# Optimization experiments

Hardware: AMD Instinct MI355X
Metric: run time of the kernel (lower is better)

## Reference

```python
import jax, jax.numpy as jnp
import numpy as np

HEADS = 12
HEAD_SIZE = 64
HIDDEN = 768


def _rope_tables(seqlen, dim, dtype):
    inv_freq = 1.0 / (10000.0 ** (jnp.arange(0, dim, 2, dtype=jnp.float32) / dim))
    t = jnp.arange(seqlen, dtype=jnp.float32)
    freqs = t[:, None] * inv_freq[None, :]  # [L, dim/2]
    return jnp.sin(freqs).astype(dtype), jnp.cos(freqs).astype(dtype)


def _apply_rope(x, sin, cos):
    # x: [B, L, H, D]; sin/cos: [L, D/2] -> broadcast as [1, L, 1, D/2]
    sin = sin[None, :, None, :]
    cos = cos[None, :, None, :]
    x1 = x[..., 0::2]
    x2 = x[..., 1::2]
    out1 = x1 * cos - x2 * sin
    out2 = x1 * sin + x2 * cos
    # interleave back: stack on new last axis then flatten
    return jnp.stack([out1, out2], axis=-1).reshape(x.shape)


def setup_inputs() -> dict:
    key = jax.random.key(0)
    k1, k2, k3 = jax.random.split(key, 3)
    B, L = 8, 512
    inputs = jax.random.normal(k1, (B, L, HIDDEN), dtype=jnp.float32)
    attention_mask = jnp.ones((B, L), dtype=jnp.int32)
    out_dim = HEADS * 2 * HEAD_SIZE
    W = jax.random.normal(k2, (HIDDEN, out_dim), dtype=jnp.float32) * (1.0 / np.sqrt(HIDDEN))
    b = jax.random.normal(k3, (out_dim,), dtype=jnp.float32) * 0.02
    return {"inputs": inputs, "W": W, "b": b, "attention_mask": attention_mask}


def reference(inputs, W, b, attention_mask):
    B, L, _ = inputs.shape
    x = inputs @ W + b  # [B, L, H*2*D]
    x = x.reshape(B, L, HEADS, 2, HEAD_SIZE)
    qw = x[..., 0, :]  # [B, L, H, D]
    kw = x[..., 1, :]
    sin, cos = _rope_tables(L, HEAD_SIZE, x.dtype)
    qw = _apply_rope(qw, sin, cos)
    kw = _apply_rope(kw, sin, cos)
    logits = jnp.einsum('bmhd,bnhd->bhmn', qw, kw) / np.sqrt(HEAD_SIZE)
    neg_inf = jnp.finfo(logits.dtype).min
    am = attention_mask.astype(bool)
    valid = am[:, None, None, :] & am[:, None, :, None]
    logits = jnp.where(valid, logits, neg_inf)
    tri = jnp.tril(jnp.ones((L, L), dtype=bool), k=-1)
    logits = jnp.where(tri[None, None, :, :], neg_inf, logits)
    return logits
```

## Files before the change

### kernel.cpp

```cpp
#include <hip/hip_runtime.h>
#include <hip/hip_bf16.h>
#include <math.h>
#include <stdint.h>

constexpr int BATCH  = 8;
constexpr int SEQ    = 512;
constexpr int HEADS  = 12;
constexpr int HSIZE  = 64;
constexpr int HIDDEN = 768;
constexpr int OUTD   = 1536;
constexpr int M      = BATCH * SEQ;
constexpr int BH     = BATCH * HEADS;

#define NEG_INF (-3.3895313892515355e38f)

typedef short  s16x8 __attribute__((ext_vector_type(8)));
typedef float  f32x4 __attribute__((ext_vector_type(4)));

__device__ __forceinline__ short f2bf(float f) {
    __hip_bfloat16 h = __float2bfloat16(f);
    return *reinterpret_cast<short*>(&h);
}

__device__ __forceinline__ void g2l16(const void* g, void* l) {
    __builtin_amdgcn_global_load_lds(
        reinterpret_cast<const __attribute__((address_space(1))) int*>(
            reinterpret_cast<uintptr_t>(g)),
        reinterpret_cast<__attribute__((address_space(3))) int*>(
            reinterpret_cast<uintptr_t>(l)),
        16, 0, 0);
}

__global__ __launch_bounds__(256) void prep_kernel(
    const float* __restrict__ X,  short* __restrict__ Xb,
    const float* __restrict__ W,  short* __restrict__ Wt,
    float* __restrict__ sc_sin,   float* __restrict__ sc_cos)
{
    __shared__ short Ls[32][36];
    const int b   = blockIdx.x;
    const int tid = threadIdx.x;

    if (b < 1536) {
        const int t = b * 256 + tid;
        const float4 a = ((const float4*)X)[t * 2];
        const float4 c = ((const float4*)X)[t * 2 + 1];
        s16x8 o;
        o[0] = f2bf(a.x); o[1] = f2bf(a.y); o[2] = f2bf(a.z); o[3] = f2bf(a.w);
        o[4] = f2bf(c.x); o[5] = f2bf(c.y); o[6] = f2bf(c.z); o[7] = f2bf(c.w);
        ((s16x8*)Xb)[t] = o;
    } else if (b < 2688) {
        const int bid = b - 1536;
        const int nx = bid % 48, ky = bid / 48;
        const int r  = tid >> 3;
        const int c4 = (tid & 7) * 4;
        const float4 v = *(const float4*)(W + (size_t)(ky * 32 + r) * OUTD + nx * 32 + c4);
        Ls[r][c4 + 0] = f2bf(v.x); Ls[r][c4 + 1] = f2bf(v.y);
        Ls[r][c4 + 2] = f2bf(v.z); Ls[r][c4 + 3] = f2bf(v.w);
        __syncthreads();
        short4 ov;
        ov.x = Ls[c4 + 0][r]; ov.y = Ls[c4 + 1][r];
        ov.z = Ls[c4 + 2][r]; ov.w = Ls[c4 + 3][r];
        *(short4*)(Wt + (size_t)(nx * 32 + r) * HIDDEN + ky * 32 + c4) = ov;
    } else {
        const int t   = (b - 2688) * 256 + tid;
        const int pos = t >> 5, pi = t & 31;
        const float invf = exp2f((float)(2 * pi) * (-13.287712379549449f / 64.0f));
        const float ang  = (float)pos * invf;
        sc_sin[t] = sinf(ang);
        sc_cos[t] = cosf(ang);
    }
}

__global__ __launch_bounds__(256) void proj_mfma_kernel(
    const short* __restrict__ Xb,
    const short* __restrict__ Wt,
    const float* __restrict__ bias,
    const float* __restrict__ sc_sin,
    const float* __restrict__ sc_cos,
    short* __restrict__ Qb,
    short* __restrict__ Kb)
{
    union Sh {
        struct { short As[2][128 * 64]; short Bs[2][64 * 64]; } st;
        float epi[128 * 68];
    };
    __shared__ Sh sh;

    const int tid = threadIdx.x;
    const int l   = tid & 63;
    const int w   = tid >> 6;

    const int f     = (blockIdx.x & 7) * 96 + (blockIdx.x >> 3);
    const int mBase = (f / 24) * 128;
    const int nBase = (f % 24) * 64;
    const int wm = w * 32;

    const int lr = l >> 3;
    const int gc = (l & 7) ^ lr;
    const short* aSrc = Xb + (size_t)(mBase + wm + lr)     * HIDDEN + gc * 8;
    const short* bSrc = Wt + (size_t)(nBase + w * 16 + lr) * HIDDEN + gc * 8;

#define STAGE(buf_, k0_)                                                     \
    do {                                                                     \
        _Pragma("unroll")                                                    \
        for (int p = 0; p < 4; ++p)                                          \
            g2l16(aSrc + (k0_) + p * 8 * HIDDEN,                             \
                  sh.st.As[buf_] + (w * 4 + p) * 512);                       \
        _Pragma("unroll")                                                    \
        for (int p = 0; p < 2; ++p)                                          \
            g2l16(bSrc + (k0_) + p * 8 * HIDDEN,                             \
                  sh.st.Bs[buf_] + (w * 2 + p) * 512);                       \
    } while (0)

    STAGE(0, 0);
    __syncthreads();

    f32x4 acc[2][4] = {};
    int buf = 0;

    for (int k0 = 0; k0 < HIDDEN; k0 += 64) {
        if (k0 + 64 < HIDDEN)
            STAGE(buf ^ 1, k0 + 64);
        const short* Asb = sh.st.As[buf];
        const short* Bsb = sh.st.Bs[buf];
#pragma unroll
        for (int s = 0; s < 2; ++s) {
            const int c = ((s * 4 + (l >> 4)) ^ (l & 7)) * 8;
            s16x8 af[2], bf[4];
#pragma unroll
            for (int i = 0; i < 2; ++i)
                af[i] = *(const s16x8*)(Asb + (wm + i * 16 + (l & 15)) * 64 + c);
#pragma unroll
            for (int j = 0; j < 4; ++j)
                bf[j] = *(const s16x8*)(Bsb + (j * 16 + (l & 15)) * 64 + c);
#pragma unroll
            for (int i = 0; i < 2; ++i)
#pragma unroll
                for (int j = 0; j < 4; ++j)
                    acc[i][j] = __builtin_amdgcn_mfma_f32_16x16x32_bf16(
                        af[i], bf[j], acc[i][j], 0, 0, 0);
        }
        __syncthreads();
        buf ^= 1;
    }
#undef STAGE

    const int colL = l & 15, quad = l >> 4;
#pragma unroll
    for (int j = 0; j < 4; ++j) {
        const int nl = j * 16 + colL;
#pragma unroll
        for (int i = 0; i < 2; ++i)
#pragma unroll
            for (int r = 0; r < 4; ++r)
                sh.epi[(wm + i * 16 + quad * 4 + r) * 68 + nl] = acc[i][j][r];
    }
    __syncthreads();

    const int bb   = mBase >> 9;
    const int pos0 = mBase & 511;
    const int h    = nBase >> 7;
    const int slot = (nBase >> 6) & 1;
    short* dst = (slot ? Kb : Qb) + ((size_t)(bb * HEADS + h) * SEQ + pos0) * HSIZE;

#pragma unroll
    for (int p = 0; p < 4; ++p) {
        const int c    = tid + p * 256;
        const int mrow = c >> 3;
        const int ch   = c & 7;
        const int dloc = ch * 8;
        const int pos  = pos0 + mrow;

        const float* src = &sh.epi[mrow * 68 + dloc];
        const float4 v0 = *(const float4*)(src);
        const float4 v1 = *(const float4*)(src + 4);
        const float* bp = bias + nBase + dloc;
        const float4 b0 = *(const float4*)(bp);
        const float4 b1 = *(const float4*)(bp + 4);
        const float4 sn = *(const float4*)(sc_sin + pos * 32 + (dloc >> 1));
        const float4 cs = *(const float4*)(sc_cos + pos * 32 + (dloc >> 1));

        const float e0 = v0.x + b0.x, o0 = v0.y + b0.y;
        const float e1 = v0.z + b0.z, o1 = v0.w + b0.w;
        const float e2 = v1.x + b1.x, o2 = v1.y + b1.y;
        const float e3 = v1.z + b1.z, o3 = v1.w + b1.w;
        s16x8 ov;
        ov[0] = f2bf(e0 * cs.x - o0 * sn.x); ov[1] = f2bf(e0 * sn.x + o0 * cs.x);
        ov[2] = f2bf(e1 * cs.y - o1 * sn.y); ov[3] = f2bf(e1 * sn.y + o1 * cs.y);
        ov[4] = f2bf(e2 * cs.z - o2 * sn.z); ov[5] = f2bf(e2 * sn.z + o2 * cs.z);
        ov[6] = f2bf(e3 * cs.w - o3 * sn.w); ov[7] = f2bf(e3 * sn.w + o3 * cs.w);
        *(s16x8*)(dst + (size_t)mrow * HSIZE + dloc) = ov;
    }
}

__global__ __launch_bounds__(256) void qk_mfma_kernel(
    const short* __restrict__ Qb,
    const short* __restrict__ Kb,
    const int*   __restrict__ am,
    float* __restrict__ out)
{
    const int t   = (blockIdx.x & 7) * 192 + (blockIdx.x >> 3);
    const int n0  = (t & 3) * 128;
    const int m0  = ((t >> 2) & 3) * 128;
    const int bh  = t >> 4;
    const int bb  = bh / HEADS;
    const int tid = threadIdx.x;

    if (m0 >= n0 + 128) {
        const float4 ninf = make_float4(NEG_INF, NEG_INF, NEG_INF, NEG_INF);
        float* base = out + ((size_t)bh * SEQ + m0) * SEQ + n0;
        const int c = (tid & 31) * 4;
#pragma unroll
        for (int r = 0; r < 16; ++r) {
            const int row = r * 8 + (tid >> 5);
            *(float4*)(base + (size_t)row * SEQ + c) = ninf;
        }
        return;
    }

    __shared__ short Qs[128 * 64];
    __shared__ short Ks[128 * 64];
    __shared__ __align__(16) int amR[128];
    __shared__ __align__(16) int amC[128];

    const int l = tid & 63;
    const int w = tid >> 6;
    if (tid < 128)      amR[tid]       = am[bb * SEQ + m0 + tid];
    else                amC[tid - 128] = am[bb * SEQ + n0 + (tid - 128)];

    const int lr = l >> 3;
    const int gc = (l & 7) ^ lr;
    const short* qSrc = Qb + ((size_t)bh * SEQ + m0 + w * 32 + lr) * HSIZE + gc * 8;
    const short* kSrc = Kb + ((size_t)bh * SEQ + n0 + w * 32 + lr) * HSIZE + gc * 8;
#pragma unroll
    for (int p = 0; p < 4; ++p) {
        g2l16(qSrc + p * 8 * HSIZE, Qs + (w * 4 + p) * 512);
        g2l16(kSrc + p * 8 * HSIZE, Ks + (w * 4 + p) * 512);
    }
    __syncthreads();

    const int wm = (w & 1) * 64;
    const int wn = (w >> 1) * 64;
    f32x4 acc[4][4] = {};
#pragma unroll
    for (int s = 0; s < 2; ++s) {
        const int c = ((s * 4 + (l >> 4)) ^ (l & 7)) * 8;
        s16x8 qf[4], kf[4];
#pragma unroll
        for (int i = 0; i < 4; ++i) {
            qf[i] = *(const s16x8*)(Qs + (wm + i * 16 + (l & 15)) * 64 + c);
            kf[i] = *(const s16x8*)(Ks + (wn + i * 16 + (l & 15)) * 64 + c);
        }
#pragma unroll
        for (int i = 0; i < 4; ++i)
#pragma unroll
            for (int j = 0; j < 4; ++j)
                acc[i][j] = __builtin_amdgcn_mfma_f32_16x16x32_bf16(
                    qf[i], kf[j], acc[i][j], 0, 0, 0);
    }

    const int colL = l & 15, quad = l >> 4;
    int rm[4][4];
#pragma unroll
    for (int i = 0; i < 4; ++i)
#pragma unroll
        for (int r = 0; r < 4; ++r)
            rm[i][r] = amR[wm + i * 16 + quad * 4 + r];

#pragma unroll
    for (int j = 0; j < 4; ++j) {
        const int nl = wn + j * 16 + colL;
        const int ng = n0 + nl;
        const int an = amC[nl];
#pragma unroll
        for (int i = 0; i < 4; ++i) {
#pragma unroll
            for (int r = 0; r < 4; ++r) {
                const int ml = wm + i * 16 + quad * 4 + r;
                const int mg = m0 + ml;
                float v = acc[i][j][r] * 0.125f;
                if (ng < mg || !an || !rm[i][r]) v = NEG_INF;
                out[((size_t)bh * SEQ + mg) * SEQ + ng] = v;
            }
        }
    }
}

extern "C" void kernel_launch(void* const* d_in, const int* in_sizes, int n_in,
                              void* d_out, int out_size, void* d_ws, size_t ws_size,
                              hipStream_t stream) {
    const float* X    = (const float*)d_in[0];
    const float* W    = (const float*)d_in[1];
    const float* bias = (const float*)d_in[2];
    const int*   am   = (const int*)d_in[3];
    float* out = (float*)d_out;

    char* ws = (char*)d_ws;
    short* Xb = (short*)(ws);
    short* Wt = (short*)(ws + 6291456);
    short* Qb = (short*)(ws + 8650752);
    short* Kb = (short*)(ws + 14942208);
    float* sc_sin = (float*)(ws + 21233664);
    float* sc_cos = (float*)(ws + 21299200);

    prep_kernel<<<dim3(2752), 256, 0, stream>>>(X, Xb, W, Wt, sc_sin, sc_cos);
    proj_mfma_kernel<<<dim3(768), 256, 0, stream>>>(
        Xb, Wt, bias, sc_sin, sc_cos, Qb, Kb);
    qk_mfma_kernel<<<dim3(1536), 256, 0, stream>>>(Qb, Kb, am, out);
}
```

Before: 140.4 us.

## Load A fragments directly from global into registers, staging only B in LDS

```diff
diff --git a/kernel.cpp b/kernel.cpp
--- a/kernel.cpp
+++ b/kernel.cpp
@@ -71,7 +71,7 @@
     }
 }
 
-__global__ __launch_bounds__(256) void proj_mfma_kernel(
+__global__ __launch_bounds__(256, 4) void proj_mfma_kernel(
     const short* __restrict__ Xb,
     const short* __restrict__ Wt,
     const float* __restrict__ bias,
@@ -81,7 +81,7 @@
     short* __restrict__ Kb)
 {
     union Sh {
-        struct { short As[2][128 * 64]; short Bs[2][64 * 64]; } st;
+        short Bs[2][64 * 64];
         float epi[128 * 68];
     };
     __shared__ Sh sh;
@@ -97,22 +97,19 @@
 
     const int lr = l >> 3;
     const int gc = (l & 7) ^ lr;
-    const short* aSrc = Xb + (size_t)(mBase + wm + lr)     * HIDDEN + gc * 8;
     const short* bSrc = Wt + (size_t)(nBase + w * 16 + lr) * HIDDEN + gc * 8;
 
-#define STAGE(buf_, k0_)                                                     \
+    const short* aRow = Xb + (size_t)(mBase + wm + (l & 15)) * HIDDEN + (l >> 4) * 8;
+
+#define STAGE_B(buf_, k0_)                                                   \
     do {                                                                     \
-        _Pragma("unroll")                                                    \
-        for (int p = 0; p < 4; ++p)                                          \
-            g2l16(aSrc + (k0_) + p * 8 * HIDDEN,                             \
-                  sh.st.As[buf_] + (w * 4 + p) * 512);                       \
         _Pragma("unroll")                                                    \
         for (int p = 0; p < 2; ++p)                                          \
             g2l16(bSrc + (k0_) + p * 8 * HIDDEN,                             \
-                  sh.st.Bs[buf_] + (w * 2 + p) * 512);                       \
+                  sh.Bs[buf_] + (w * 2 + p) * 512);                          \
     } while (0)
 
-    STAGE(0, 0);
+    STAGE_B(0, 0);
     __syncthreads();
 
     f32x4 acc[2][4] = {};
@@ -120,30 +117,36 @@
 
     for (int k0 = 0; k0 < HIDDEN; k0 += 64) {
         if (k0 + 64 < HIDDEN)
-            STAGE(buf ^ 1, k0 + 64);
-        const short* Asb = sh.st.As[buf];
-        const short* Bsb = sh.st.Bs[buf];
+            STAGE_B(buf ^ 1, k0 + 64);
+
+        s16x8 a00 = *(const s16x8*)(aRow + k0);
+        s16x8 a10 = *(const s16x8*)(aRow + 16 * HIDDEN + k0);
+        s16x8 a01 = *(const s16x8*)(aRow + k0 + 32);
+        s16x8 a11 = *(const s16x8*)(aRow + 16 * HIDDEN + k0 + 32);
+
+        const short* Bsb = sh.Bs[buf];
 #pragma unroll
         for (int s = 0; s < 2; ++s) {
             const int c = ((s * 4 + (l >> 4)) ^ (l & 7)) * 8;
-            s16x8 af[2], bf[4];
-#pragma unroll
-            for (int i = 0; i < 2; ++i)
-                af[i] = *(const s16x8*)(Asb + (wm + i * 16 + (l & 15)) * 64 + c);
+            s16x8 bf[4];
 #pragma unroll
             for (int j = 0; j < 4; ++j)
                 bf[j] = *(const s16x8*)(Bsb + (j * 16 + (l & 15)) * 64 + c);
-#pragma unroll
-            for (int i = 0; i < 2; ++i)
-#pragma unroll
-                for (int j = 0; j < 4; ++j)
-                    acc[i][j] = __builtin_amdgcn_mfma_f32_16x16x32_bf16(
-                        af[i], bf[j], acc[i][j], 0, 0, 0);
+            const s16x8 a0 = s ? a01 : a00;
+            const s16x8 a1 = s ? a11 : a10;
+#pragma unroll
+            for (int j = 0; j < 4; ++j)
+                acc[0][j] = __builtin_amdgcn_mfma_f32_16x16x32_bf16(
+                    a0, bf[j], acc[0][j], 0, 0, 0);
+#pragma unroll
+            for (int j = 0; j < 4; ++j)
+                acc[1][j] = __builtin_amdgcn_mfma_f32_16x16x32_bf16(
+                    a1, bf[j], acc[1][j], 0, 0, 0);
         }
         __syncthreads();
         buf ^= 1;
     }
-#undef STAGE
+#undef STAGE_B
 
     const int colL = l & 15, quad = l >> 4;
 #pragma unroll
```

After: 149.2 us. 6.3% more time.
